# Kernel tuning notes

Hardware: AMD Instinct MI355X
Metric: run time of the kernel (lower is better)

## Reference

```python
import jax, jax.numpy as jnp
import numpy as np


def setup_inputs() -> dict:
    key = jax.random.key(0)
    kq, kk, kv = jax.random.split(key, 3)
    B, L, H, D = 2, 4096, 8, 64
    queries = jax.random.normal(kq, (B, L, H, D), dtype=jnp.float32)
    keys = jax.random.normal(kk, (B, L, H, D), dtype=jnp.float32)
    values = jax.random.normal(kv, (B, L, H, D), dtype=jnp.float32)
    return {"queries": queries, "keys": keys, "values": values}


def reference(queries, keys, values):
    # queries/keys/values: [B, L, H, D]
    d_model = queries.shape[-1]
    scale = 1.0 / jnp.sqrt(jnp.asarray(d_model, dtype=queries.dtype))
    # scores: [B, H, Lq, Lk]
    scores = jnp.einsum('blhd,bshd->bhls', queries, keys)
    # dropout is identity in eval mode / for deterministic reference
    A = jax.nn.softmax(scale * scores, axis=-1)
    # output: [B, Lq, H, D]
    V = jnp.einsum('bhls,bshd->blhd', A, values)
    return V
```

## Files before the change

### kernel.cpp

```cpp
#include <hip/hip_runtime.h>

#define Bn 2
#define Ln 4096
#define Hn 8
#define Dn 64
#define NMEGA 32
#define BH_STRIDE 262144

typedef float    f32x4  __attribute__((ext_vector_type(4)));
typedef float    f32x16 __attribute__((ext_vector_type(16)));
typedef _Float16 f16x2  __attribute__((ext_vector_type(2)));
typedef _Float16 f16x8  __attribute__((ext_vector_type(8)));
typedef unsigned int u32;
typedef u32 u32x2 __attribute__((ext_vector_type(2)));
typedef u32 u32x4 __attribute__((ext_vector_type(4)));

static __device__ __forceinline__ u32 pkf16(float a, float b){
    auto h = __builtin_amdgcn_cvt_pkrtz(a, b);
    return __builtin_bit_cast(u32, h);
}

static __device__ __forceinline__ u32x2 swp(u32 a, u32 b){
    auto r = __builtin_amdgcn_permlane32_swap(a, b, false, false);
    return __builtin_bit_cast(u32x2, r);
}

__global__ __launch_bounds__(256)
void kvprep(const float* __restrict__ Kg, const float* __restrict__ Vg,
            _Float16* __restrict__ kp, _Float16* __restrict__ vp){
    const int t2 = blockIdx.x, bh = blockIdx.y, b = bh>>3, h = bh&7;
    const int tid = threadIdx.x;
    const int w = tid >> 6, lane = tid & 63;
    const int l31 = lane & 31, hi = lane >> 5;
    const int t = t2 >> 1, g = t2 & 1;
    _Float16* outbase = (_Float16*)((char*)0) ;
    (void)outbase;

    {
        const float* ks = Kg + (((size_t)b*Ln + t2*32 + l31)*Hn + h)*Dn + w*16 + hi*8;
        float4 a  = *(const float4*)ks;
        float4 c4 = *(const float4*)(ks + 4);
        f16x8 o;
        o[0]=(_Float16)a.x;  o[1]=(_Float16)a.y;  o[2]=(_Float16)a.z;  o[3]=(_Float16)a.w;
        o[4]=(_Float16)c4.x; o[5]=(_Float16)c4.y; o[6]=(_Float16)c4.z; o[7]=(_Float16)c4.w;
        *(f16x8*)(kp + (size_t)bh*BH_STRIDE + (size_t)t*4096
                     + (size_t)(g*4 + w)*512 + (size_t)lane*8) = o;
    }

    {
        const int kh = w >> 1, dt = w & 1;
        const float* vs = Vg + (((size_t)b*Ln + t2*32 + kh*16 + hi*8)*Hn + h)*Dn
                        + dt*32 + l31;
        f16x8 o;
#pragma unroll
        for(int j=0;j<8;++j) o[j] = (_Float16)vs[(size_t)j*Hn*Dn];
        *(f16x8*)(vp + (size_t)bh*BH_STRIDE + (size_t)t*4096
                     + (size_t)(g*4 + w)*512 + (size_t)lane*8) = o;
    }
}

static __device__ __forceinline__ f32x16 qk4(const f16x8 (&kf)[4], const f16x8 (&qf)[4]){
    f32x16 s;
#pragma unroll
    for(int r=0;r<16;++r) s[r]=0.f;
    s = __builtin_amdgcn_mfma_f32_32x32x16_f16(kf[0], qf[0], s, 0,0,0);
    s = __builtin_amdgcn_mfma_f32_32x32x16_f16(kf[1], qf[1], s, 0,0,0);
    s = __builtin_amdgcn_mfma_f32_32x32x16_f16(kf[2], qf[2], s, 0,0,0);
    s = __builtin_amdgcn_mfma_f32_32x32x16_f16(kf[3], qf[3], s, 0,0,0);
    return s;
}

static __device__ __forceinline__ void finish_pv(const f32x16& S, float& lac,
                                                 f32x16& o0, f32x16& o1,
                                                 const f16x8 (&vf)[4]){
    f32x16 p;
#pragma unroll
    for(int r=0;r<16;++r) p[r] = __builtin_amdgcn_exp2f(S[r]);
    u32 A0 = pkf16(p[0],p[1]),   A1 = pkf16(p[2],p[3]);
    u32 B0 = pkf16(p[4],p[5]),   B1 = pkf16(p[6],p[7]);
    u32 C0 = pkf16(p[8],p[9]),   C1 = pkf16(p[10],p[11]);
    u32 D0 = pkf16(p[12],p[13]), D1 = pkf16(p[14],p[15]);
    u32x2 r0 = swp(A0,B0), r1 = swp(A1,B1);
    u32x2 r2 = swp(C0,D0), r3 = swp(C1,D1);
    u32x4 w0 = {r0.x, r1.x, r0.y, r1.y};
    u32x4 w1 = {r2.x, r3.x, r2.y, r3.y};
    f16x8 pa0 = __builtin_bit_cast(f16x8, w0);
    f16x8 pa1 = __builtin_bit_cast(f16x8, w1);
    const f16x2 ones = {(_Float16)1.0f, (_Float16)1.0f};
#pragma unroll
    for(int j=0;j<4;++j){
        f16x2 c0 = {pa0[2*j], pa0[2*j+1]};
        f16x2 c1 = {pa1[2*j], pa1[2*j+1]};
        lac = __builtin_amdgcn_fdot2(c0, ones, lac, false);
        lac = __builtin_amdgcn_fdot2(c1, ones, lac, false);
    }
    o0 = __builtin_amdgcn_mfma_f32_32x32x16_f16(pa0, vf[0], o0, 0,0,0);
    o0 = __builtin_amdgcn_mfma_f32_32x32x16_f16(pa1, vf[2], o0, 0,0,0);
    o1 = __builtin_amdgcn_mfma_f32_32x32x16_f16(pa0, vf[1], o1, 0,0,0);
    o1 = __builtin_amdgcn_mfma_f32_32x32x16_f16(pa1, vf[3], o1, 0,0,0);
}

static __device__ __forceinline__ void ld4(f16x8 (&dst)[4], const char* base, int off){
#pragma unroll
    for(int i=0;i<4;++i) dst[i] = *(const f16x8*)(base + ((off+i)<<10));
}

__global__ __launch_bounds__(256,2)
void attn_fwd(const float* __restrict__ Qg, float* __restrict__ Og,
              const _Float16* __restrict__ kp, const _Float16* __restrict__ vp){
    __shared__ __align__(16) float xo[128*68 + 128];

    const int tid  = threadIdx.x;
    const int lane = tid & 63, wv = tid >> 6;
    const int qh = wv & 1, kh2 = wv >> 1;
    const int l31 = lane & 31, hi = lane >> 5;
    const int bh = blockIdx.x, b = bh>>3, h = bh&7;
    const int q0 = blockIdx.y*128 + qh*64;

    const float c = 0.125f * 1.4426950408889634f;

    f16x8 qf[2][4];
#pragma unroll
    for(int qt=0;qt<2;++qt){
        const float* qrow = Qg + (((size_t)b*Ln + q0 + qt*32 + l31)*Hn + h)*Dn;
#pragma unroll
        for(int cc=0;cc<4;++cc){
            const float* p4 = qrow + cc*16 + hi*8;
            float4 x = *(const float4*)p4;
            float4 y = *(const float4*)(p4+4);
            f16x8 f;
            f[0]=(_Float16)(x.x*c); f[1]=(_Float16)(x.y*c);
            f[2]=(_Float16)(x.z*c); f[3]=(_Float16)(x.w*c);
            f[4]=(_Float16)(y.x*c); f[5]=(_Float16)(y.y*c);
            f[6]=(_Float16)(y.z*c); f[7]=(_Float16)(y.w*c);
            qf[qt][cc]=f;
        }
    }

    f32x16 o[2][2];
    float lac[2] = {0.f, 0.f};
#pragma unroll
    for(int qt=0;qt<2;++qt)
#pragma unroll
        for(int dt=0;dt<2;++dt)
#pragma unroll
            for(int r=0;r<16;++r) o[qt][dt][r]=0.f;

    const char* kgc = (const char*)(kp + (size_t)bh*BH_STRIDE) + kh2*8192 + lane*16;
    const char* vgc = (const char*)(vp + (size_t)bh*BH_STRIDE) + kh2*8192 + lane*16;

    for(int T=0; T<NMEGA; ++T){
        const char* Kb = kgc + (size_t)T*16384;
        const char* Vb = vgc + (size_t)T*16384;

        f16x8 kf0[4], vf0[4];
        ld4(kf0, Kb, 0); ld4(vf0, Vb, 0);

        f32x16 S0 = qk4(kf0, qf[0]);
        f32x16 S1 = qk4(kf0, qf[1]);

        f16x8 kf1[4], vf1[4];
        ld4(kf1, Kb, 4); ld4(vf1, Vb, 4);

        finish_pv(S0, lac[0], o[0][0], o[0][1], vf0);
        f32x16 S0b = qk4(kf1, qf[0]);
        finish_pv(S1, lac[1], o[1][0], o[1][1], vf0);
        f32x16 S1b = qk4(kf1, qf[1]);
        finish_pv(S0b, lac[0], o[0][0], o[0][1], vf1);
        finish_pv(S1b, lac[1], o[1][0], o[1][1], vf1);
    }

    float lred[2];
#pragma unroll
    for(int qt=0;qt<2;++qt)
        lred[qt] = lac[qt] + __shfl_xor(lac[qt], 32, 64);

    float* xl = xo + 128*68;
    if(kh2){
#pragma unroll
        for(int qt=0;qt<2;++qt){
#pragma unroll
            for(int dt=0;dt<2;++dt)
#pragma unroll
                for(int r=0;r<16;++r){
                    int qr = (r&3) + 8*(r>>2) + 4*hi;
                    xo[(qh*64 + qt*32 + qr)*68 + dt*32 + l31] = o[qt][dt][r];
                }
            if(hi==0) xl[qh*64 + qt*32 + l31] = lred[qt];
        }
    }
    __syncthreads();
    if(!kh2){
#pragma unroll
        for(int qt=0;qt<2;++qt){
            float inv = 1.0f/(lred[qt] + xl[qh*64 + qt*32 + l31]);
            float* ob = Og + (((size_t)b*Ln + q0 + qt*32)*Hn + h)*Dn;
#pragma unroll
            for(int r=0;r<16;++r){
                int qr = (r&3) + 8*(r>>2) + 4*hi;
                float invr = __shfl(inv, qr, 64);
#pragma unroll
                for(int dt=0;dt<2;++dt){
                    float val = o[qt][dt][r] + xo[(qh*64 + qt*32 + qr)*68 + dt*32 + l31];
                    ob[(size_t)qr*Hn*Dn + dt*32 + l31] = val*invr;
                }
            }
        }
    }
}

extern "C" void kernel_launch(void* const* d_in, const int* in_sizes, int n_in,
                              void* d_out, int out_size, void* d_ws, size_t ws_size,
                              hipStream_t stream) {
    const float* Q = (const float*)d_in[0];
    const float* K = (const float*)d_in[1];
    const float* V = (const float*)d_in[2];
    float* O = (float*)d_out;

    _Float16* kp = (_Float16*)d_ws;
    _Float16* vp = (_Float16*)((char*)d_ws + (8u<<20));

    kvprep<<<dim3(128, 16), dim3(256), 0, stream>>>(K, V, kp, vp);
    attn_fwd<<<dim3(16, 32), dim3(256), 0, stream>>>(Q, O, kp, vp);
}
```

Baseline: 162.3 us.

## Split key range four ways per block and halve query tile per block

Each block now handles 64 queries instead of 128, with all four waves sharing the same query rows and each wave taking a quarter of the key sequence. Partial outputs and row sums are reduced through shared memory in two stages before the final normalization and store. This doubles the grid to 1024 blocks for better CU occupancy and load balance, and shortens each wave's per-iteration work. In exchange, each block re-reads all of K and V for fewer queries, which doubles global traffic for K/V, and the reduction adds extra syncs and LDS traffic.

```diff
diff --git a/kernel.cpp b/kernel.cpp
--- a/kernel.cpp
+++ b/kernel.cpp
@@ -33,8 +33,6 @@
     const int w = tid >> 6, lane = tid & 63;
     const int l31 = lane & 31, hi = lane >> 5;
     const int t = t2 >> 1, g = t2 & 1;
-    _Float16* outbase = (_Float16*)((char*)0) ;
-    (void)outbase;
 
     {
         const float* ks = Kg + (((size_t)b*Ln + t2*32 + l31)*Hn + h)*Dn + w*16 + hi*8;
@@ -100,22 +98,22 @@
     o1 = __builtin_amdgcn_mfma_f32_32x32x16_f16(pa1, vf[3], o1, 0,0,0);
 }
 
-static __device__ __forceinline__ void ld4(f16x8 (&dst)[4], const char* base, int off){
-#pragma unroll
-    for(int i=0;i<4;++i) dst[i] = *(const f16x8*)(base + ((off+i)<<10));
+static __device__ __forceinline__ void ld4(f16x8 (&dst)[4], const char* base){
+#pragma unroll
+    for(int i=0;i<4;++i) dst[i] = *(const f16x8*)(base + (i<<10));
 }
 
 __global__ __launch_bounds__(256,2)
 void attn_fwd(const float* __restrict__ Qg, float* __restrict__ Og,
               const _Float16* __restrict__ kp, const _Float16* __restrict__ vp){
-    __shared__ __align__(16) float xo[128*68 + 128];
+    __shared__ __align__(16) float xo[8320];
 
     const int tid  = threadIdx.x;
     const int lane = tid & 63, wv = tid >> 6;
-    const int qh = wv & 1, kh2 = wv >> 1;
+    const int kh2 = wv >> 1, g = wv & 1;
     const int l31 = lane & 31, hi = lane >> 5;
     const int bh = blockIdx.x, b = bh>>3, h = bh&7;
-    const int q0 = blockIdx.y*128 + qh*64;
+    const int q0 = blockIdx.y*64;
 
     const float c = 0.125f * 1.4426950408889634f;
 
@@ -146,28 +144,21 @@
 #pragma unroll
             for(int r=0;r<16;++r) o[qt][dt][r]=0.f;
 
-    const char* kgc = (const char*)(kp + (size_t)bh*BH_STRIDE) + kh2*8192 + lane*16;
-    const char* vgc = (const char*)(vp + (size_t)bh*BH_STRIDE) + kh2*8192 + lane*16;
+    const int sub = kh2*8192 + g*4096 + lane*16;
+    const char* kgc = (const char*)(kp + (size_t)bh*BH_STRIDE) + sub;
+    const char* vgc = (const char*)(vp + (size_t)bh*BH_STRIDE) + sub;
 
     for(int T=0; T<NMEGA; ++T){
         const char* Kb = kgc + (size_t)T*16384;
         const char* Vb = vgc + (size_t)T*16384;
 
-        f16x8 kf0[4], vf0[4];
-        ld4(kf0, Kb, 0); ld4(vf0, Vb, 0);
-
-        f32x16 S0 = qk4(kf0, qf[0]);
-        f32x16 S1 = qk4(kf0, qf[1]);
-
-        f16x8 kf1[4], vf1[4];
-        ld4(kf1, Kb, 4); ld4(vf1, Vb, 4);
-
-        finish_pv(S0, lac[0], o[0][0], o[0][1], vf0);
-        f32x16 S0b = qk4(kf1, qf[0]);
-        finish_pv(S1, lac[1], o[1][0], o[1][1], vf0);
-        f32x16 S1b = qk4(kf1, qf[1]);
-        finish_pv(S0b, lac[0], o[0][0], o[0][1], vf1);
-        finish_pv(S1b, lac[1], o[1][0], o[1][1], vf1);
+        f16x8 kf[4], vf[4];
+        ld4(kf, Kb); ld4(vf, Vb);
+
+        f32x16 S0 = qk4(kf, qf[0]);
+        f32x16 S1 = qk4(kf, qf[1]);
+        finish_pv(S0, lac[0], o[0][0], o[0][1], vf);
+        finish_pv(S1, lac[1], o[1][0], o[1][1], vf);
     }
 
     float lred[2];
@@ -175,8 +166,14 @@
     for(int qt=0;qt<2;++qt)
         lred[qt] = lac[qt] + __shfl_xor(lac[qt], 32, 64);
 
-    float* xl = xo + 128*68;
-    if(kh2){
+    float* xb0 = xo;
+    float* xb1 = xo + 4096;
+    float* xl0 = xo + 8192;
+    float* xl1 = xo + 8256;
+
+    if(g==1){
+        float* xb = kh2 ? xb1 : xb0;
+        float* xl = kh2 ? xl1 : xl0;
 #pragma unroll
         for(int qt=0;qt<2;++qt){
 #pragma unroll
@@ -184,26 +181,55 @@
 #pragma unroll
                 for(int r=0;r<16;++r){
                     int qr = (r&3) + 8*(r>>2) + 4*hi;
-                    xo[(qh*64 + qt*32 + qr)*68 + dt*32 + l31] = o[qt][dt][r];
+                    xb[(qt*32 + qr)*64 + dt*32 + l31] = o[qt][dt][r];
                 }
-            if(hi==0) xl[qh*64 + qt*32 + l31] = lred[qt];
+            if(hi==0) xl[qt*32 + l31] = lred[qt];
         }
     }
     __syncthreads();
-    if(!kh2){
-#pragma unroll
-        for(int qt=0;qt<2;++qt){
-            float inv = 1.0f/(lred[qt] + xl[qh*64 + qt*32 + l31]);
+    if(g==0){
+        float* xb = kh2 ? xb1 : xb0;
+        float* xl = kh2 ? xl1 : xl0;
+#pragma unroll
+        for(int qt=0;qt<2;++qt){
+#pragma unroll
+            for(int dt=0;dt<2;++dt)
+#pragma unroll
+                for(int r=0;r<16;++r){
+                    int qr = (r&3) + 8*(r>>2) + 4*hi;
+                    o[qt][dt][r] += xb[(qt*32 + qr)*64 + dt*32 + l31];
+                }
+            lred[qt] += xl[qt*32 + l31];
+        }
+    }
+    __syncthreads();
+    if(wv==2){
+#pragma unroll
+        for(int qt=0;qt<2;++qt){
+#pragma unroll
+            for(int dt=0;dt<2;++dt)
+#pragma unroll
+                for(int r=0;r<16;++r){
+                    int qr = (r&3) + 8*(r>>2) + 4*hi;
+                    xb0[(qt*32 + qr)*64 + dt*32 + l31] = o[qt][dt][r];
+                }
+            if(hi==0) xl0[qt*32 + l31] = lred[qt];
+        }
+    }
+    __syncthreads();
+    if(wv==0){
+#pragma unroll
+        for(int qt=0;qt<2;++qt){
+            float inv = 1.0f/(lred[qt] + xl0[qt*32 + l31]);
             float* ob = Og + (((size_t)b*Ln + q0 + qt*32)*Hn + h)*Dn;
 #pragma unroll
             for(int r=0;r<16;++r){
                 int qr = (r&3) + 8*(r>>2) + 4*hi;
                 float invr = __shfl(inv, qr, 64);
-#pragma unroll
-                for(int dt=0;dt<2;++dt){
-                    float val = o[qt][dt][r] + xo[(qh*64 + qt*32 + qr)*68 + dt*32 + l31];
-                    ob[(size_t)qr*Hn*Dn + dt*32 + l31] = val*invr;
-                }
+                float v0 = o[qt][0][r] + xb0[(qt*32 + qr)*64 +  0 + l31];
+                float v1 = o[qt][1][r] + xb0[(qt*32 + qr)*64 + 32 + l31];
+                ob[(size_t)qr*Hn*Dn +  0 + l31] = v0*invr;
+                ob[(size_t)qr*Hn*Dn + 32 + l31] = v1*invr;
             }
         }
     }
@@ -221,5 +247,5 @@
     _Float16* vp = (_Float16*)((char*)d_ws + (8u<<20));
 
     kvprep<<<dim3(128, 16), dim3(256), 0, stream>>>(K, V, kp, vp);
-    attn_fwd<<<dim3(16, 32), dim3(256), 0, stream>>>(Q, O, kp, vp);
-}
+    attn_fwd<<<dim3(16, 64), dim3(256), 0, stream>>>(Q, O, kp, vp);
+}
```

Result: slower. 168.5 us (+3.8%).
